# Kernel tuning notes

Hardware: AMD Instinct MI355X
Metric: run time of the kernel (lower is better)

## Reference

```python
import jax, jax.numpy as jnp
import numpy as np

B, T, D = 32, 512, 256
F = 256  # duration_predictor_filter_size
K = 3    # kernel size, padding=1
MEL_MAX = 2304
EPS = 1e-5


def _conv1d(x, w, b):
    # x: [B, T, C_in], w: [C_out, C_in, K], 'same'-ish padding=1
    y = jax.lax.conv_general_dilated(
        x.transpose(0, 2, 1), w, window_strides=(1,), padding=[(1, 1)],
        dimension_numbers=("NCH", "OIH", "NCH"))
    return y.transpose(0, 2, 1) + b


def _layernorm(x, g, b):
    mu = jnp.mean(x, axis=-1, keepdims=True)
    var = jnp.mean(jnp.square(x - mu), axis=-1, keepdims=True)
    return (x - mu) * jax.lax.rsqrt(var + EPS) * g + b


def setup_inputs() -> dict:
    key = jax.random.key(0)
    ks = jax.random.split(key, 8)
    x = jax.random.normal(ks[0], (B, T, D), dtype=jnp.float32)
    target = jax.random.randint(ks[1], (B, T), 0, 8, dtype=jnp.int32)
    s = 0.02
    return {
        "x": x,
        "target": target,
        "mel_max_length": MEL_MAX,
        "conv1_w": jax.random.normal(ks[2], (F, D, K), dtype=jnp.float32) * s,
        "conv1_b": jnp.zeros((F,), jnp.float32),
        "ln1_g": jnp.ones((F,), jnp.float32),
        "ln1_b": jnp.zeros((F,), jnp.float32),
        "conv2_w": jax.random.normal(ks[3], (F, F, K), dtype=jnp.float32) * s,
        "conv2_b": jnp.zeros((F,), jnp.float32),
        "ln2_g": jnp.ones((F,), jnp.float32),
        "ln2_b": jnp.zeros((F,), jnp.float32),
        "lin_w": jax.random.normal(ks[4], (1, F), dtype=jnp.float32) * s,
        "lin_b": jnp.zeros((1,), jnp.float32),
    }


def reference(x, target, mel_max_length, conv1_w, conv1_b, ln1_g, ln1_b,
              conv2_w, conv2_b, ln2_g, ln2_b, lin_w, lin_b):
    # Variance_adaptor (duration predictor), eval-mode dropout = identity
    h = jax.nn.relu(_layernorm(_conv1d(x, conv1_w, conv1_b), ln1_g, ln1_b))
    h = jax.nn.relu(_layernorm(_conv1d(h, conv2_w, conv2_b), ln2_g, ln2_b))
    dur_pred = jax.nn.relu(jnp.einsum("btf,of->bto", h, lin_w) + lin_b)[..., 0]  # [B,T]

    # LR: alignment @ x, expressed as the equivalent duration-indexed gather.
    # alignment[b, t_out, j] = 1 iff cumsum(dur)[b,j-1] <= t_out < cumsum(dur)[b,j]
    cum = jnp.cumsum(target, axis=1)                    # [B, T]
    t_out = jnp.arange(mel_max_length, dtype=cum.dtype)  # [T_out]
    idx = jax.vmap(lambda c: jnp.searchsorted(c, t_out, side="right"))(cum)  # [B, T_out]
    valid = (t_out[None, :] < cum[:, -1:]).astype(x.dtype)                   # [B, T_out]
    gathered = jnp.take_along_axis(x, jnp.clip(idx, 0, T - 1)[:, :, None], axis=1)
    output = gathered * valid[:, :, None]                # zeros past total length (pad)
    return output, dur_pred
```

## Files before the change

kernel.cpp:

```cpp
#include <hip/hip_runtime.h>

typedef __attribute__((ext_vector_type(8))) short short8;
typedef __attribute__((ext_vector_type(4))) float floatx4;
typedef __attribute__((ext_vector_type(4))) float f4v;

typedef __attribute__((address_space(3))) unsigned int lds_u32;
typedef __attribute__((address_space(1))) const unsigned int glb_u32;

static __device__ __forceinline__ unsigned short f2bf(float f) {
    unsigned int u = __float_as_uint(f);
    return (unsigned short)((u + 0x7FFFu + ((u >> 16) & 1u)) >> 16);
}
static __device__ __forceinline__ void cp16(const ushort* g, ushort* l) {
    __builtin_amdgcn_global_load_lds((glb_u32*)g, (lds_u32*)l, 16, 0, 0);
}


__global__ __launch_bounds__(256)
void prep_kernel(const float* __restrict__ x, const int* __restrict__ target,
                 const float* __restrict__ w1, const float* __restrict__ w2,
                 ushort* __restrict__ xb, ushort* __restrict__ h1b,
                 ushort* __restrict__ w1q, ushort* __restrict__ w2q,
                 int* __restrict__ cumg)
{
    __shared__ int ps[256];
    const int blk = blockIdx.x, tid = threadIdx.x;
    if (blk < 4112) {
        const int r = blk * 4 + (tid >> 6);
        const int c = (tid & 63) * 4;
        const int b = r / 514, tp = r % 514;
        const int e2 = ((((c >> 3) ^ (tp & 7)) << 3) | (c & 7));
        ushort4 o;
        if (tp >= 1 && tp <= 512) {
            float4 v = *(const float4*)(x + ((size_t)(b * 512 + tp - 1) * 256 + c));
            o.x = f2bf(v.x); o.y = f2bf(v.y); o.z = f2bf(v.z); o.w = f2bf(v.w);
        } else {
            o.x = o.y = o.z = o.w = 0;
            *(ushort4*)(h1b + (size_t)r * 256 + e2) = o;
        }
        *(ushort4*)(xb + (size_t)r * 256 + e2) = o;
    } else if (blk < 5648) {
        const bool second = blk >= 4880;
        const int e = (blk - (second ? 4880 : 4112)) * 256 + tid;
        const float* w = second ? w2 : w1;
        ushort* wq = second ? w2q : w1q;
        const int f = e / 768, j = e % 768;
        const int c = j & 255, kr = j >> 8;
        const int se = kr * 4 + (c >> 6);
        const int kk = c & 63;
        const int wg = f >> 6, ni = (f >> 4) & 3, colf = f & 15;
        const int kh = kk >> 5, qk = (kk >> 3) & 3, jj = kk & 7;
        wq[(size_t)se * 16384 + wg * 4096 + (ni * 2 + kh) * 512
           + (qk * 16 + colf) * 8 + jj] = f2bf(w[f * 768 + c * 3 + kr]);
    } else {
        const int b = blk - 5648;
        const int v0 = target[b * 512 + 2 * tid];
        const int v1 = target[b * 512 + 2 * tid + 1];
        ps[tid] = v0 + v1;
        __syncthreads();
        for (int off = 1; off < 256; off <<= 1) {
            int t = (tid >= off) ? ps[tid - off] : 0;
            __syncthreads();
            ps[tid] += t;
            __syncthreads();
        }
        const int excl = tid ? ps[tid - 1] : 0;
        cumg[b * 512 + 2 * tid]     = excl + v0;
        cumg[b * 512 + 2 * tid + 1] = excl + v0 + v1;
    }
}

template<bool IS_CONV2>
__global__ __launch_bounds__(256, 3)
void conv_mfma_kernel(const ushort* __restrict__ src,
                      const ushort* __restrict__ wq,
                      const float* __restrict__ cbias,
                      const float* __restrict__ gamma, const float* __restrict__ beta,
                      const float* __restrict__ lw, const float* __restrict__ lb,
                      ushort* __restrict__ outb,
                      float* __restrict__ durp,
                      const float* __restrict__ x,
                      const int* __restrict__ cumg,
                      float* __restrict__ out0,
                      int gbase)
{
    __shared__ ushort slab[36 * 256];
    __shared__ float sum_s[4][32], sq_s[4][32], mu_s[32], rs_s[32];
    __shared__ int cum_s[512], sidx[64];

    const int tid = threadIdx.x;
    const int grp = blockIdx.x / 17, rmod = blockIdx.x % 17;

    if (rmod >= 8) {
        const int bg = gbase + grp * 9 + (rmod - 8);
        const int b = bg / 36, t0o = (bg % 36) * 64;
        cum_s[tid]       = cumg[b * 512 + tid];
        cum_s[tid + 256] = cumg[b * 512 + 256 + tid];
        __syncthreads();
        const int total = cum_s[511];
        if (tid < 64) {
            int t = t0o + tid;
            int lo = 0, hi = 512;
            while (lo < hi) {
                int mid = (lo + hi) >> 1;
                if (cum_s[mid] <= t) lo = mid + 1; else hi = mid;
            }
            sidx[tid] = (t < total) ? ((lo < 512) ? lo : 511) : -1;
        }
        __syncthreads();
        const f4v* x4 = (const f4v*)x;
        f4v* o4 = (f4v*)out0;
        const int lane6 = tid & 63, g4 = tid >> 6;
        #pragma unroll 4
        for (int rr = 0; rr < 16; ++rr) {
            int r = rr * 4 + g4;
            int idx = sidx[r];
            f4v v = {0.f, 0.f, 0.f, 0.f};
            if (idx >= 0) v = x4[((size_t)(b * 512 + idx)) * 64 + lane6];
            __builtin_nontemporal_store(v, &o4[((size_t)(b * 2304 + t0o + r)) * 64 + lane6]);
        }
        return;
    }
    const int conv_id = grp * 8 + rmod;

    const int w_ = tid >> 6, lane = tid & 63;
    const int q = lane >> 4, col = lane & 15;
    const int b  = conv_id & 31;
    const int t0 = (conv_id >> 5) << 5;
    const int rot = conv_id % 12;

    const ushort* xbb = src + (size_t)b * 514 * 256;
    #pragma unroll
    for (int r = 0; r < 4; ++r) {
        const int i = r * 8 + w_ * 2 + (lane >> 5);
        cp16(xbb + (size_t)(t0 + i) * 256 + (lane & 31) * 8,
             slab + r * 2048 + w_ * 512);
    }
    if (w_ < 2) {
        const int i = 32 + w_ * 2 + (lane >> 5);
        cp16(xbb + (size_t)(t0 + i) * 256 + (lane & 31) * 8,
             slab + 8192 + w_ * 512);
    }
    __syncthreads();

    floatx4 acc[2][4] = {};
    const ushort* bptr = wq + (size_t)w_ * 4096 + lane * 8;
    #pragma unroll
    for (int s = 0; s < 12; ++s) {
        int se = s + rot; if (se >= 12) se -= 12;
        const int krow = se >> 2, cb8 = (se & 3) << 3;
        short8 bf[4][2], af[2][2];
        #pragma unroll
        for (int ni = 0; ni < 4; ++ni)
            #pragma unroll
            for (int kh = 0; kh < 2; ++kh)
                bf[ni][kh] = *(const short8*)(bptr + (size_t)se * 16384 + (ni * 2 + kh) * 512);
        #pragma unroll
        for (int mi = 0; mi < 2; ++mi) {
            #pragma unroll
            for (int kh = 0; kh < 2; ++kh) {
                const int i = krow + mi * 16 + col;
                const int ch = cb8 + kh * 4 + q;
                af[mi][kh] = *(const short8*)(slab + i * 256 + ((ch ^ (i & 7)) << 3));
            }
        }
        #pragma unroll
        for (int kh = 0; kh < 2; ++kh)
            #pragma unroll
            for (int mi = 0; mi < 2; ++mi)
                #pragma unroll
                for (int ni = 0; ni < 4; ++ni)
                    acc[mi][ni] = __builtin_amdgcn_mfma_f32_16x16x32_bf16(
                        af[mi][kh], bf[ni][kh], acc[mi][ni], 0, 0, 0);
    }

    const int base_c = w_ * 64;
    float cb4[4], gm4[4], bt4[4];
    #pragma unroll
    for (int ni = 0; ni < 4; ++ni) {
        cb4[ni] = cbias[base_c + ni * 16 + col];
        gm4[ni] = gamma[base_c + ni * 16 + col];
        bt4[ni] = beta [base_c + ni * 16 + col];
    }
    float rsum[2][4] = {}, rsq[2][4] = {};
    #pragma unroll
    for (int mi = 0; mi < 2; ++mi)
        #pragma unroll
        for (int ni = 0; ni < 4; ++ni)
            #pragma unroll
            for (int r = 0; r < 4; ++r) {
                float v = acc[mi][ni][r] + cb4[ni];
                acc[mi][ni][r] = v;
                rsum[mi][r] += v;
                rsq [mi][r] += v * v;
            }
    #pragma unroll
    for (int mi = 0; mi < 2; ++mi)
        #pragma unroll
        for (int r = 0; r < 4; ++r) {
            float s = rsum[mi][r], ss = rsq[mi][r];
            #pragma unroll
            for (int d = 8; d > 0; d >>= 1) {
                s  += __shfl_down(s,  d, 16);
                ss += __shfl_down(ss, d, 16);
            }
            if (col == 0) {
                sum_s[w_][mi * 16 + q * 4 + r] = s;
                sq_s [w_][mi * 16 + q * 4 + r] = ss;
            }
        }
    __syncthreads();
    if (tid < 32) {
        float s  = sum_s[0][tid] + sum_s[1][tid] + sum_s[2][tid] + sum_s[3][tid];
        float ss = sq_s [0][tid] + sq_s [1][tid] + sq_s [2][tid] + sq_s [3][tid];
        float mu = s * (1.f / 256.f);
        mu_s[tid] = mu;
        rs_s[tid] = rsqrtf(ss * (1.f / 256.f) - mu * mu + 1e-5f);
    }
    __syncthreads();

    if (!IS_CONV2) {
        #pragma unroll
        for (int mi = 0; mi < 2; ++mi)
            #pragma unroll
            for (int ni = 0; ni < 4; ++ni)
                #pragma unroll
                for (int r = 0; r < 4; ++r) {
                    int row = mi * 16 + q * 4 + r;
                    float v = (acc[mi][ni][r] - mu_s[row]) * rs_s[row] * gm4[ni] + bt4[ni];
                    const int tp = t0 + row + 1;
                    const int cc = base_c + ni * 16 + col;
                    const int e2 = ((((cc >> 3) ^ (tp & 7)) << 3) | (cc & 7));
                    outb[((size_t)b * 514 + tp) * 256 + e2] = f2bf(fmaxf(v, 0.f));
                }
    } else {
        float lw4[4];
        #pragma unroll
        for (int ni = 0; ni < 4; ++ni) lw4[ni] = lw[base_c + ni * 16 + col];
        float dsum[2][4] = {};
        #pragma unroll
        for (int mi = 0; mi < 2; ++mi)
            #pragma unroll
            for (int ni = 0; ni < 4; ++ni)
                #pragma unroll
                for (int r = 0; r < 4; ++r) {
                    int row = mi * 16 + q * 4 + r;
                    float v = (acc[mi][ni][r] - mu_s[row]) * rs_s[row] * gm4[ni] + bt4[ni];
                    dsum[mi][r] += fmaxf(v, 0.f) * lw4[ni];
                }
        #pragma unroll
        for (int mi = 0; mi < 2; ++mi)
            #pragma unroll
            for (int r = 0; r < 4; ++r) {
                float s = dsum[mi][r];
                #pragma unroll
                for (int d = 8; d > 0; d >>= 1) s += __shfl_down(s, d, 16);
                if (col == 0) sum_s[w_][mi * 16 + q * 4 + r] = s;
            }
        __syncthreads();
        if (tid < 32)
            durp[b * 512 + t0 + tid] = fmaxf(sum_s[0][tid] + sum_s[1][tid]
                                           + sum_s[2][tid] + sum_s[3][tid] + lb[0], 0.f);
    }
}

extern "C" void kernel_launch(void* const* d_in, const int* in_sizes, int n_in,
                              void* d_out, int out_size, void* d_ws, size_t ws_size,
                              hipStream_t stream) {
    const float* x      = (const float*)d_in[0];
    const int*   target = (const int*)  d_in[1];
    const float* c1w = (const float*)d_in[3];
    const float* c1b = (const float*)d_in[4];
    const float* g1  = (const float*)d_in[5];
    const float* b1  = (const float*)d_in[6];
    const float* c2w = (const float*)d_in[7];
    const float* c2b = (const float*)d_in[8];
    const float* g2  = (const float*)d_in[9];
    const float* b2  = (const float*)d_in[10];
    const float* lw  = (const float*)d_in[11];
    const float* lb  = (const float*)d_in[12];

    const size_t PADEL = (size_t)32 * 514 * 256;
    ushort* xb   = (ushort*)d_ws;
    ushort* h1b  = xb + PADEL;
    ushort* w1q  = h1b + PADEL;
    ushort* w2q  = w1q + 196608;
    int*    cumg = (int*)(w2q + 196608);

    float* out0 = (float*)d_out;
    float* durp = out0 + (size_t)32 * 2304 * 256;

    prep_kernel<<<5680, 256, 0, stream>>>(x, target, c1w, c2w, xb, h1b, w1q, w2q, cumg);
    conv_mfma_kernel<false><<<1088, 256, 0, stream>>>(
        xb, w1q, c1b, g1, b1, nullptr, nullptr, h1b, nullptr,
        x, cumg, out0, 0);
    conv_mfma_kernel<true><<<1088, 256, 0, stream>>>(
        h1b, w2q, c2b, g2, b2, lw, lb, nullptr, durp,
        x, cumg, out0, 576);
}
```

Before: 150.7 us.

## Fuse both conv layers into one kernel with halo recompute in LDS

Merges the two conv+layernorm stages into a single kernel. Each block converts its fp32 x rows (with a 2-row halo) to bf16 straight into LDS, computes conv1 over 48 rows, keeps h1 in LDS, then computes conv2 and the duration head. This removes the padded bf16 x and h1 round trips through global memory, the prep conversion pass and one kernel launch. In exchange it recomputes halo rows of conv1 (48 rows per 32 outputs), uses more LDS and registers with occupancy dropped to 2, and replaces the async global-to-LDS copy with register-staged loads.

```diff
diff --git a/kernel.cpp b/kernel.cpp
--- a/kernel.cpp
+++ b/kernel.cpp
@@ -3,45 +3,23 @@
 typedef __attribute__((ext_vector_type(8))) short short8;
 typedef __attribute__((ext_vector_type(4))) float floatx4;
 typedef __attribute__((ext_vector_type(4))) float f4v;
-
-typedef __attribute__((address_space(3))) unsigned int lds_u32;
-typedef __attribute__((address_space(1))) const unsigned int glb_u32;
 
 static __device__ __forceinline__ unsigned short f2bf(float f) {
     unsigned int u = __float_as_uint(f);
     return (unsigned short)((u + 0x7FFFu + ((u >> 16) & 1u)) >> 16);
 }
-static __device__ __forceinline__ void cp16(const ushort* g, ushort* l) {
-    __builtin_amdgcn_global_load_lds((glb_u32*)g, (lds_u32*)l, 16, 0, 0);
-}
-
 
 __global__ __launch_bounds__(256)
-void prep_kernel(const float* __restrict__ x, const int* __restrict__ target,
+void prep_kernel(const int* __restrict__ target,
                  const float* __restrict__ w1, const float* __restrict__ w2,
-                 ushort* __restrict__ xb, ushort* __restrict__ h1b,
                  ushort* __restrict__ w1q, ushort* __restrict__ w2q,
                  int* __restrict__ cumg)
 {
     __shared__ int ps[256];
     const int blk = blockIdx.x, tid = threadIdx.x;
-    if (blk < 4112) {
-        const int r = blk * 4 + (tid >> 6);
-        const int c = (tid & 63) * 4;
-        const int b = r / 514, tp = r % 514;
-        const int e2 = ((((c >> 3) ^ (tp & 7)) << 3) | (c & 7));
-        ushort4 o;
-        if (tp >= 1 && tp <= 512) {
-            float4 v = *(const float4*)(x + ((size_t)(b * 512 + tp - 1) * 256 + c));
-            o.x = f2bf(v.x); o.y = f2bf(v.y); o.z = f2bf(v.z); o.w = f2bf(v.w);
-        } else {
-            o.x = o.y = o.z = o.w = 0;
-            *(ushort4*)(h1b + (size_t)r * 256 + e2) = o;
-        }
-        *(ushort4*)(xb + (size_t)r * 256 + e2) = o;
-    } else if (blk < 5648) {
-        const bool second = blk >= 4880;
-        const int e = (blk - (second ? 4880 : 4112)) * 256 + tid;
+    if (blk < 1536) {
+        const bool second = blk >= 768;
+        const int e = (blk - (second ? 768 : 0)) * 256 + tid;
         const float* w = second ? w2 : w1;
         ushort* wq = second ? w2q : w1q;
         const int f = e / 768, j = e % 768;
@@ -53,7 +31,7 @@
         wq[(size_t)se * 16384 + wg * 4096 + (ni * 2 + kh) * 512
            + (qk * 16 + colf) * 8 + jj] = f2bf(w[f * 768 + c * 3 + kr]);
     } else {
-        const int b = blk - 5648;
+        const int b = blk - 1536;
         const int v0 = target[b * 512 + 2 * tid];
         const int v1 = target[b * 512 + 2 * tid + 1];
         ps[tid] = v0 + v1;
@@ -70,42 +48,46 @@
     }
 }
 
-template<bool IS_CONV2>
-__global__ __launch_bounds__(256, 3)
-void conv_mfma_kernel(const ushort* __restrict__ src,
-                      const ushort* __restrict__ wq,
-                      const float* __restrict__ cbias,
-                      const float* __restrict__ gamma, const float* __restrict__ beta,
-                      const float* __restrict__ lw, const float* __restrict__ lb,
-                      ushort* __restrict__ outb,
-                      float* __restrict__ durp,
-                      const float* __restrict__ x,
-                      const int* __restrict__ cumg,
-                      float* __restrict__ out0,
-                      int gbase)
+__global__ __launch_bounds__(256, 2)
+void fused_kernel(const float* __restrict__ x,
+                  const ushort* __restrict__ w1q,
+                  const ushort* __restrict__ w2q,
+                  const float* __restrict__ c1b, const float* __restrict__ g1,
+                  const float* __restrict__ b1,
+                  const float* __restrict__ c2b, const float* __restrict__ g2,
+                  const float* __restrict__ b2,
+                  const float* __restrict__ lw, const float* __restrict__ lb,
+                  const int* __restrict__ cumg,
+                  float* __restrict__ out0,
+                  float* __restrict__ durp)
 {
-    __shared__ ushort slab[36 * 256];
-    __shared__ float sum_s[4][32], sq_s[4][32], mu_s[32], rs_s[32];
-    __shared__ int cum_s[512], sidx[64];
+    __shared__ union {
+        struct {
+            ushort xs[50 * 256];
+            ushort hl[48 * 256];
+            float sum_s[4][48], sq_s[4][48], mu_s[48], rs_s[48];
+        } c;
+        struct { int cum[512]; int sidx[64]; } g;
+    } sh;
 
     const int tid = threadIdx.x;
-    const int grp = blockIdx.x / 17, rmod = blockIdx.x % 17;
-
-    if (rmod >= 8) {
-        const int bg = gbase + grp * 9 + (rmod - 8);
+    const int grp = blockIdx.x / 13, rmod = blockIdx.x % 13;
+
+    if (rmod >= 4) {
+        const int bg = grp * 9 + (rmod - 4);
         const int b = bg / 36, t0o = (bg % 36) * 64;
-        cum_s[tid]       = cumg[b * 512 + tid];
-        cum_s[tid + 256] = cumg[b * 512 + 256 + tid];
-        __syncthreads();
-        const int total = cum_s[511];
+        sh.g.cum[tid]       = cumg[b * 512 + tid];
+        sh.g.cum[tid + 256] = cumg[b * 512 + 256 + tid];
+        __syncthreads();
+        const int total = sh.g.cum[511];
         if (tid < 64) {
             int t = t0o + tid;
             int lo = 0, hi = 512;
             while (lo < hi) {
                 int mid = (lo + hi) >> 1;
-                if (cum_s[mid] <= t) lo = mid + 1; else hi = mid;
-            }
-            sidx[tid] = (t < total) ? ((lo < 512) ? lo : 511) : -1;
+                if (sh.g.cum[mid] <= t) lo = mid + 1; else hi = mid;
+            }
+            sh.g.sidx[tid] = (t < total) ? ((lo < 512) ? lo : 511) : -1;
         }
         __syncthreads();
         const f4v* x4 = (const f4v*)x;
@@ -114,153 +96,238 @@
         #pragma unroll 4
         for (int rr = 0; rr < 16; ++rr) {
             int r = rr * 4 + g4;
-            int idx = sidx[r];
+            int idx = sh.g.sidx[r];
             f4v v = {0.f, 0.f, 0.f, 0.f};
             if (idx >= 0) v = x4[((size_t)(b * 512 + idx)) * 64 + lane6];
             __builtin_nontemporal_store(v, &o4[((size_t)(b * 2304 + t0o + r)) * 64 + lane6]);
         }
         return;
     }
-    const int conv_id = grp * 8 + rmod;
-
+
+    const int conv_id = grp * 4 + rmod;
     const int w_ = tid >> 6, lane = tid & 63;
     const int q = lane >> 4, col = lane & 15;
     const int b  = conv_id & 31;
     const int t0 = (conv_id >> 5) << 5;
     const int rot = conv_id % 12;
 
-    const ushort* xbb = src + (size_t)b * 514 * 256;
-    #pragma unroll
-    for (int r = 0; r < 4; ++r) {
-        const int i = r * 8 + w_ * 2 + (lane >> 5);
-        cp16(xbb + (size_t)(t0 + i) * 256 + (lane & 31) * 8,
-             slab + r * 2048 + w_ * 512);
-    }
-    if (w_ < 2) {
-        const int i = 32 + w_ * 2 + (lane >> 5);
-        cp16(xbb + (size_t)(t0 + i) * 256 + (lane & 31) * 8,
-             slab + 8192 + w_ * 512);
+    {
+        const float* xb_ = x + (size_t)b * 512 * 256;
+        #pragma unroll
+        for (int r7 = 0; r7 < 7; ++r7) {
+            const int id = r7 * 256 + tid;
+            if (id < 1600) {
+                const int lr = id >> 5, ch = id & 31;
+                const int xrow = t0 - 2 + lr;
+                float4 v0 = make_float4(0.f, 0.f, 0.f, 0.f), v1 = v0;
+                if (xrow >= 0 && xrow < 512) {
+                    const float* px = xb_ + ((size_t)xrow * 256 + ch * 8);
+                    v0 = *(const float4*)px;
+                    v1 = *(const float4*)(px + 4);
+                }
+                short8 o;
+                o[0] = f2bf(v0.x); o[1] = f2bf(v0.y); o[2] = f2bf(v0.z); o[3] = f2bf(v0.w);
+                o[4] = f2bf(v1.x); o[5] = f2bf(v1.y); o[6] = f2bf(v1.z); o[7] = f2bf(v1.w);
+                *(short8*)(sh.c.xs + lr * 256 + ((ch ^ (lr & 7)) << 3)) = o;
+            }
+        }
     }
     __syncthreads();
 
-    floatx4 acc[2][4] = {};
-    const ushort* bptr = wq + (size_t)w_ * 4096 + lane * 8;
-    #pragma unroll
-    for (int s = 0; s < 12; ++s) {
-        int se = s + rot; if (se >= 12) se -= 12;
-        const int krow = se >> 2, cb8 = (se & 3) << 3;
-        short8 bf[4][2], af[2][2];
-        #pragma unroll
-        for (int ni = 0; ni < 4; ++ni)
-            #pragma unroll
-            for (int kh = 0; kh < 2; ++kh)
-                bf[ni][kh] = *(const short8*)(bptr + (size_t)se * 16384 + (ni * 2 + kh) * 512);
-        #pragma unroll
-        for (int mi = 0; mi < 2; ++mi) {
-            #pragma unroll
-            for (int kh = 0; kh < 2; ++kh) {
-                const int i = krow + mi * 16 + col;
-                const int ch = cb8 + kh * 4 + q;
-                af[mi][kh] = *(const short8*)(slab + i * 256 + ((ch ^ (i & 7)) << 3));
-            }
-        }
-        #pragma unroll
-        for (int kh = 0; kh < 2; ++kh)
-            #pragma unroll
-            for (int mi = 0; mi < 2; ++mi)
-                #pragma unroll
-                for (int ni = 0; ni < 4; ++ni)
-                    acc[mi][ni] = __builtin_amdgcn_mfma_f32_16x16x32_bf16(
-                        af[mi][kh], bf[ni][kh], acc[mi][ni], 0, 0, 0);
+    floatx4 a1[3][4] = {};
+    {
+        const ushort* b1p = w1q + (size_t)w_ * 4096 + lane * 8;
+        #pragma unroll
+        for (int s = 0; s < 12; ++s) {
+            int se = s + rot; if (se >= 12) se -= 12;
+            const int kr = se >> 2, cb8 = (se & 3) << 3;
+            short8 bf[4][2];
+            #pragma unroll
+            for (int ni = 0; ni < 4; ++ni)
+                #pragma unroll
+                for (int kh = 0; kh < 2; ++kh)
+                    bf[ni][kh] = *(const short8*)(b1p + (size_t)se * 16384 + (ni * 2 + kh) * 512);
+            #pragma unroll
+            for (int mt = 0; mt < 3; ++mt) {
+                short8 af[2];
+                #pragma unroll
+                for (int kh = 0; kh < 2; ++kh) {
+                    const int xl = mt * 16 + col + kr;
+                    const int ch = cb8 + kh * 4 + q;
+                    af[kh] = *(const short8*)(sh.c.xs + xl * 256 + ((ch ^ (xl & 7)) << 3));
+                }
+                #pragma unroll
+                for (int kh = 0; kh < 2; ++kh)
+                    #pragma unroll
+                    for (int ni = 0; ni < 4; ++ni)
+                        a1[mt][ni] = __builtin_amdgcn_mfma_f32_16x16x32_bf16(
+                            af[kh], bf[ni][kh], a1[mt][ni], 0, 0, 0);
+            }
+        }
     }
 
     const int base_c = w_ * 64;
-    float cb4[4], gm4[4], bt4[4];
-    #pragma unroll
-    for (int ni = 0; ni < 4; ++ni) {
-        cb4[ni] = cbias[base_c + ni * 16 + col];
-        gm4[ni] = gamma[base_c + ni * 16 + col];
-        bt4[ni] = beta [base_c + ni * 16 + col];
-    }
-    float rsum[2][4] = {}, rsq[2][4] = {};
-    #pragma unroll
-    for (int mi = 0; mi < 2; ++mi)
-        #pragma unroll
-        for (int ni = 0; ni < 4; ++ni)
+    {
+        float cb4[4], gm4[4], bt4[4];
+        #pragma unroll
+        for (int ni = 0; ni < 4; ++ni) {
+            cb4[ni] = c1b[base_c + ni * 16 + col];
+            gm4[ni] = g1 [base_c + ni * 16 + col];
+            bt4[ni] = b1 [base_c + ni * 16 + col];
+        }
+        float rsum[3][4] = {}, rsq[3][4] = {};
+        #pragma unroll
+        for (int mt = 0; mt < 3; ++mt)
+            #pragma unroll
+            for (int ni = 0; ni < 4; ++ni)
+                #pragma unroll
+                for (int r = 0; r < 4; ++r) {
+                    float v = a1[mt][ni][r] + cb4[ni];
+                    a1[mt][ni][r] = v;
+                    rsum[mt][r] += v;
+                    rsq [mt][r] += v * v;
+                }
+        #pragma unroll
+        for (int mt = 0; mt < 3; ++mt)
             #pragma unroll
             for (int r = 0; r < 4; ++r) {
-                float v = acc[mi][ni][r] + cb4[ni];
-                acc[mi][ni][r] = v;
-                rsum[mi][r] += v;
-                rsq [mi][r] += v * v;
-            }
-    #pragma unroll
-    for (int mi = 0; mi < 2; ++mi)
-        #pragma unroll
-        for (int r = 0; r < 4; ++r) {
-            float s = rsum[mi][r], ss = rsq[mi][r];
-            #pragma unroll
-            for (int d = 8; d > 0; d >>= 1) {
-                s  += __shfl_down(s,  d, 16);
-                ss += __shfl_down(ss, d, 16);
-            }
-            if (col == 0) {
-                sum_s[w_][mi * 16 + q * 4 + r] = s;
-                sq_s [w_][mi * 16 + q * 4 + r] = ss;
-            }
-        }
+                float s = rsum[mt][r], ss = rsq[mt][r];
+                #pragma unroll
+                for (int d = 8; d > 0; d >>= 1) {
+                    s  += __shfl_down(s,  d, 16);
+                    ss += __shfl_down(ss, d, 16);
+                }
+                if (col == 0) {
+                    sh.c.sum_s[w_][mt * 16 + q * 4 + r] = s;
+                    sh.c.sq_s [w_][mt * 16 + q * 4 + r] = ss;
+                }
+            }
+        __syncthreads();
+        if (tid < 48) {
+            float s  = sh.c.sum_s[0][tid] + sh.c.sum_s[1][tid] + sh.c.sum_s[2][tid] + sh.c.sum_s[3][tid];
+            float ss = sh.c.sq_s [0][tid] + sh.c.sq_s [1][tid] + sh.c.sq_s [2][tid] + sh.c.sq_s [3][tid];
+            float mu = s * (1.f / 256.f);
+            sh.c.mu_s[tid] = mu;
+            sh.c.rs_s[tid] = rsqrtf(ss * (1.f / 256.f) - mu * mu + 1e-5f);
+        }
+        __syncthreads();
+        #pragma unroll
+        for (int mt = 0; mt < 3; ++mt)
+            #pragma unroll
+            for (int ni = 0; ni < 4; ++ni)
+                #pragma unroll
+                for (int r = 0; r < 4; ++r) {
+                    const int row = mt * 16 + q * 4 + r;
+                    const int tabs = t0 - 1 + row;
+                    float v = (a1[mt][ni][r] - sh.c.mu_s[row]) * sh.c.rs_s[row] * gm4[ni] + bt4[ni];
+                    ushort u = (tabs >= 0 && tabs < 512) ? f2bf(fmaxf(v, 0.f)) : (ushort)0;
+                    const int chunk = w_ * 8 + ni * 2 + (col >> 3);
+                    sh.c.hl[row * 256 + (((chunk ^ (row & 7)) << 3) | (col & 7))] = u;
+                }
+    }
     __syncthreads();
-    if (tid < 32) {
-        float s  = sum_s[0][tid] + sum_s[1][tid] + sum_s[2][tid] + sum_s[3][tid];
-        float ss = sq_s [0][tid] + sq_s [1][tid] + sq_s [2][tid] + sq_s [3][tid];
-        float mu = s * (1.f / 256.f);
-        mu_s[tid] = mu;
-        rs_s[tid] = rsqrtf(ss * (1.f / 256.f) - mu * mu + 1e-5f);
-    }
-    __syncthreads();
-
-    if (!IS_CONV2) {
-        #pragma unroll
-        for (int mi = 0; mi < 2; ++mi)
+
+    floatx4 a2[2][4] = {};
+    {
+        const ushort* b2p = w2q + (size_t)w_ * 4096 + lane * 8;
+        #pragma unroll
+        for (int s = 0; s < 12; ++s) {
+            int se = s + rot; if (se >= 12) se -= 12;
+            const int kr = se >> 2, cb8 = (se & 3) << 3;
+            short8 bf[4][2];
+            #pragma unroll
+            for (int ni = 0; ni < 4; ++ni)
+                #pragma unroll
+                for (int kh = 0; kh < 2; ++kh)
+                    bf[ni][kh] = *(const short8*)(b2p + (size_t)se * 16384 + (ni * 2 + kh) * 512);
+            #pragma unroll
+            for (int mt = 0; mt < 2; ++mt) {
+                short8 af[2];
+                #pragma unroll
+                for (int kh = 0; kh < 2; ++kh) {
+                    const int h2 = mt * 16 + col + kr;
+                    const int ch = cb8 + kh * 4 + q;
+                    af[kh] = *(const short8*)(sh.c.hl + h2 * 256 + ((ch ^ (h2 & 7)) << 3));
+                }
+                #pragma unroll
+                for (int kh = 0; kh < 2; ++kh)
+                    #pragma unroll
+                    for (int ni = 0; ni < 4; ++ni)
+                        a2[mt][ni] = __builtin_amdgcn_mfma_f32_16x16x32_bf16(
+                            af[kh], bf[ni][kh], a2[mt][ni], 0, 0, 0);
+            }
+        }
+    }
+
+    {
+        float cb4[4], gm4[4], bt4[4], lw4[4];
+        #pragma unroll
+        for (int ni = 0; ni < 4; ++ni) {
+            cb4[ni] = c2b[base_c + ni * 16 + col];
+            gm4[ni] = g2 [base_c + ni * 16 + col];
+            bt4[ni] = b2 [base_c + ni * 16 + col];
+            lw4[ni] = lw [base_c + ni * 16 + col];
+        }
+        float rsum[2][4] = {}, rsq[2][4] = {};
+        #pragma unroll
+        for (int mt = 0; mt < 2; ++mt)
             #pragma unroll
             for (int ni = 0; ni < 4; ++ni)
                 #pragma unroll
                 for (int r = 0; r < 4; ++r) {
-                    int row = mi * 16 + q * 4 + r;
-                    float v = (acc[mi][ni][r] - mu_s[row]) * rs_s[row] * gm4[ni] + bt4[ni];
-                    const int tp = t0 + row + 1;
-                    const int cc = base_c + ni * 16 + col;
-                    const int e2 = ((((cc >> 3) ^ (tp & 7)) << 3) | (cc & 7));
-                    outb[((size_t)b * 514 + tp) * 256 + e2] = f2bf(fmaxf(v, 0.f));
-                }
-    } else {
-        float lw4[4];
-        #pragma unroll
-        for (int ni = 0; ni < 4; ++ni) lw4[ni] = lw[base_c + ni * 16 + col];
+                    float v = a2[mt][ni][r] + cb4[ni];
+                    a2[mt][ni][r] = v;
+                    rsum[mt][r] += v;
+                    rsq [mt][r] += v * v;
+                }
+        #pragma unroll
+        for (int mt = 0; mt < 2; ++mt)
+            #pragma unroll
+            for (int r = 0; r < 4; ++r) {
+                float s = rsum[mt][r], ss = rsq[mt][r];
+                #pragma unroll
+                for (int d = 8; d > 0; d >>= 1) {
+                    s  += __shfl_down(s,  d, 16);
+                    ss += __shfl_down(ss, d, 16);
+                }
+                if (col == 0) {
+                    sh.c.sum_s[w_][mt * 16 + q * 4 + r] = s;
+                    sh.c.sq_s [w_][mt * 16 + q * 4 + r] = ss;
+                }
+            }
+        __syncthreads();
+        if (tid < 32) {
+            float s  = sh.c.sum_s[0][tid] + sh.c.sum_s[1][tid] + sh.c.sum_s[2][tid] + sh.c.sum_s[3][tid];
+            float ss = sh.c.sq_s [0][tid] + sh.c.sq_s [1][tid] + sh.c.sq_s [2][tid] + sh.c.sq_s [3][tid];
+            float mu = s * (1.f / 256.f);
+            sh.c.mu_s[tid] = mu;
+            sh.c.rs_s[tid] = rsqrtf(ss * (1.f / 256.f) - mu * mu + 1e-5f);
+        }
+        __syncthreads();
         float dsum[2][4] = {};
         #pragma unroll
-        for (int mi = 0; mi < 2; ++mi)
+        for (int mt = 0; mt < 2; ++mt)
             #pragma unroll
             for (int ni = 0; ni < 4; ++ni)
                 #pragma unroll
                 for (int r = 0; r < 4; ++r) {
-                    int row = mi * 16 + q * 4 + r;
-                    float v = (acc[mi][ni][r] - mu_s[row]) * rs_s[row] * gm4[ni] + bt4[ni];
-                    dsum[mi][r] += fmaxf(v, 0.f) * lw4[ni];
-                }
-        #pragma unroll
-        for (int mi = 0; mi < 2; ++mi)
+                    const int row = mt * 16 + q * 4 + r;
+                    float v = (a2[mt][ni][r] - sh.c.mu_s[row]) * sh.c.rs_s[row] * gm4[ni] + bt4[ni];
+                    dsum[mt][r] += fmaxf(v, 0.f) * lw4[ni];
+                }
+        #pragma unroll
+        for (int mt = 0; mt < 2; ++mt)
             #pragma unroll
             for (int r = 0; r < 4; ++r) {
-                float s = dsum[mi][r];
+                float s = dsum[mt][r];
                 #pragma unroll
                 for (int d = 8; d > 0; d >>= 1) s += __shfl_down(s, d, 16);
-                if (col == 0) sum_s[w_][mi * 16 + q * 4 + r] = s;
+                if (col == 0) sh.c.sum_s[w_][mt * 16 + q * 4 + r] = s;
             }
         __syncthreads();
         if (tid < 32)
-            durp[b * 512 + t0 + tid] = fmaxf(sum_s[0][tid] + sum_s[1][tid]
-                                           + sum_s[2][tid] + sum_s[3][tid] + lb[0], 0.f);
+            durp[b * 512 + t0 + tid] = fmaxf(sh.c.sum_s[0][tid] + sh.c.sum_s[1][tid]
+                                           + sh.c.sum_s[2][tid] + sh.c.sum_s[3][tid] + lb[0], 0.f);
     }
 }
 
@@ -280,21 +347,14 @@
     const float* lw  = (const float*)d_in[11];
     const float* lb  = (const float*)d_in[12];
 
-    const size_t PADEL = (size_t)32 * 514 * 256;
-    ushort* xb   = (ushort*)d_ws;
-    ushort* h1b  = xb + PADEL;
-    ushort* w1q  = h1b + PADEL;
+    ushort* w1q  = (ushort*)d_ws;
     ushort* w2q  = w1q + 196608;
     int*    cumg = (int*)(w2q + 196608);
 
     float* out0 = (float*)d_out;
     float* durp = out0 + (size_t)32 * 2304 * 256;
 
-    prep_kernel<<<5680, 256, 0, stream>>>(x, target, c1w, c2w, xb, h1b, w1q, w2q, cumg);
-    conv_mfma_kernel<false><<<1088, 256, 0, stream>>>(
-        xb, w1q, c1b, g1, b1, nullptr, nullptr, h1b, nullptr,
-        x, cumg, out0, 0);
-    conv_mfma_kernel<true><<<1088, 256, 0, stream>>>(
-        h1b, w2q, c2b, g2, b2, lw, lb, nullptr, durp,
-        x, cumg, out0, 576);
+    prep_kernel<<<1568, 256, 0, stream>>>(target, c1w, c2w, w1q, w2q, cumg);
+    fused_kernel<<<1664, 256, 0, stream>>>(
+        x, w1q, w2q, c1b, g1, b1, c2b, g2, b2, lw, lb, cumg, out0, durp);
 }
```

After: 158.3 us. 1.05x slower.
